# Kernel optimization log

Measured on AMD Instinct MI355X. Metric: run time of the kernel, lower is better.

## Reference

```python
import jax, jax.numpy as jnp
import numpy as np

D_MODEL = 1024
N_HEADS = 16
D_K = D_MODEL // N_HEADS  # 64
SCALE = 0.125             # attention_scale = 1/sqrt(d_k)
ROPE_BASE = 10000.0
NEG_INF = -1e30


def setup_inputs() -> dict:
    key = jax.random.key(0)
    k1, k2, k3 = jax.random.split(key, 3)
    B, S = 2, 2048
    x = jax.random.normal(k1, (B, S, D_MODEL), jnp.float32)
    # torch Linear(d_model, 3*d_model, bias=False): stored here as [in, out]
    w_qkv = jax.random.normal(k2, (D_MODEL, 3 * D_MODEL), jnp.float32) * (D_MODEL ** -0.5)
    w_o = jax.random.normal(k3, (D_MODEL, D_MODEL), jnp.float32) * (D_MODEL ** -0.5)
    return {"x": x, "w_qkv": w_qkv, "w_o": w_o}


def _rotary(x):
    # x: [B, H, S, D]; standard half-split rotary over sequence positions
    S, D = x.shape[2], x.shape[3]
    inv_freq = 1.0 / (ROPE_BASE ** (jnp.arange(0, D, 2, dtype=jnp.float32) / D))  # [D/2]
    freqs = jnp.arange(S, dtype=jnp.float32)[:, None] * inv_freq[None, :]          # [S, D/2]
    cos = jnp.cos(freqs)[None, None]  # [1,1,S,D/2]
    sin = jnp.sin(freqs)[None, None]
    x1, x2 = jnp.split(x, 2, axis=-1)
    return jnp.concatenate([x1 * cos + x2 * sin, -x1 * sin + x2 * cos], axis=-1).astype(x.dtype)


def reference(x, w_qkv, w_o):
    B, S, _ = x.shape
    qkv = x @ w_qkv                                        # [B,S,3*D_MODEL]
    qkv = qkv.reshape(B, S, 3, N_HEADS, D_K).transpose(2, 0, 3, 1, 4)  # [3,B,H,S,Dk]
    q, k, v = qkv[0], qkv[1], qkv[2]
    q = _rotary(q)
    k = _rotary(k)
    scores = jnp.einsum('bhqd,bhkd->bhqk', q, k) * SCALE   # [B,H,S,S]
    causal = jnp.tril(jnp.ones((S, S), dtype=bool))
    scores = jnp.where(causal, scores, NEG_INF)
    attn = jax.nn.softmax(scores, axis=-1)
    out = jnp.einsum('bhqk,bhkd->bhqd', attn, v)           # [B,H,S,Dk]
    out = out.transpose(0, 2, 1, 3).reshape(B, S, D_MODEL)
    return out @ w_o
```

## Files before the change

### kernel.cpp

```cpp
#include <hip/hip_runtime.h>

typedef short bf16x8 __attribute__((ext_vector_type(8)));
typedef short bf16x4 __attribute__((ext_vector_type(4)));
typedef float f32x4 __attribute__((ext_vector_type(4)));
typedef float f32x16 __attribute__((ext_vector_type(16)));
typedef int i32x4 __attribute__((ext_vector_type(4)));

#define DEVI static __device__ __forceinline__

DEVI unsigned short f2b(float f) {
  unsigned u = __float_as_uint(f);
  u += 0x7FFFu + ((u >> 16) & 1u);
  return (unsigned short)(u >> 16);
}

DEVI void gload16(const void* g, void* l) {
  __builtin_amdgcn_global_load_lds((const __attribute__((address_space(1))) void*)g,
                                   (__attribute__((address_space(3))) void*)l, 16, 0, 0);
}

DEVI void pl32swap(int a, int b, int& outa, int& outb) {
#if __has_builtin(__builtin_amdgcn_permlane32_swap)
  auto r = __builtin_amdgcn_permlane32_swap(a, b, false, false);
  outa = ((const int*)&r)[0];
  outb = ((const int*)&r)[1];
#else
  int bp = __shfl_xor(b, 32);
  int ap = __shfl_xor(a, 32);
  outa = (threadIdx.x & 32) ? bp : a;
  outb = (threadIdx.x & 32) ? b : ap;
#endif
}

DEVI float halfmax(float x) {
  int o0, o1;
  pl32swap(__float_as_int(x), __float_as_int(x), o0, o1);
  return fmaxf(__int_as_float(o0), __int_as_float(o1));
}
DEVI float halfsum(float x) {
  int o0, o1;
  pl32swap(__float_as_int(x), __float_as_int(x), o0, o1);
  return __int_as_float(o0) + __int_as_float(o1);
}

__global__ void rope_table_kernel(float2* __restrict__ cst) {
  int i = blockIdx.x * 256 + threadIdx.x;
  int s = i >> 5, j = i & 31;
  float inv = powf(10000.0f, -(float)j * (1.0f / 32.0f));
  float a = (float)s * inv;
  cst[i] = make_float2(cosf(a), sinf(a));
}

__global__ void cvt_x_kernel(const float* __restrict__ x, unsigned short* __restrict__ xb) {
  int i = blockIdx.x * 256 + threadIdx.x;
  float4 v = ((const float4*)x)[i];
  ushort4 o;
  o.x = f2b(v.x); o.y = f2b(v.y); o.z = f2b(v.z); o.w = f2b(v.w);
  ((ushort4*)xb)[i] = o;
}

__global__ void transpose2_kernel(const float* __restrict__ W1, unsigned short* __restrict__ WT1,
                                  const float* __restrict__ W2, unsigned short* __restrict__ WT2) {
  __shared__ float tile[32][33];
  int bx = blockIdx.x;
  const float* W; unsigned short* WT; int N;
  if (bx < 96) { W = W1; WT = WT1; N = 3072; }
  else         { W = W2; WT = WT2; N = 1024; bx -= 96; }
  const int K = 1024;
  int n0 = bx * 32, k0 = blockIdx.y * 32;
  int tx = threadIdx.x, ty = threadIdx.y;
#pragma unroll
  for (int i = 0; i < 32; i += 8)
    tile[ty + i][tx] = W[(size_t)(k0 + ty + i) * N + n0 + tx];
  __syncthreads();
#pragma unroll
  for (int i = 0; i < 32; i += 8)
    WT[(size_t)(n0 + ty + i) * K + k0 + tx] = f2b(tile[tx][ty + i]);
}

DEVI void gemm_mainloop(const unsigned short* __restrict__ A, const unsigned short* __restrict__ B,
                        unsigned short* As, unsigned short* Bs,
                        int m0, int n0, int lane, int wid, int wr, int wc,
                        f32x4 acc[4][4]) {
  const int srow = lane >> 3;
  const int scc = ((lane & 7) ^ srow) * 8;
  const int rx = lane & 7;
  auto stage = [&](int k0, int nb) {
    unsigned short* Ad = As + nb * 8192;
    unsigned short* Bd = Bs + nb * 8192;
#pragma unroll
    for (int i = 0; i < 4; ++i) {
      const int c = i * 4 + wid;
      const int row = c * 8 + srow;
      gload16(A + (size_t)(m0 + row) * 1024 + k0 + scc, (char*)Ad + c * 1024);
      gload16(B + (size_t)(n0 + row) * 1024 + k0 + scc, (char*)Bd + c * 1024);
    }
  };
  auto compute = [&](int nb) {
    const unsigned short* Ab = As + nb * 8192;
    const unsigned short* Bb = Bs + nb * 8192;
#pragma unroll
    for (int kk = 0; kk < 64; kk += 32) {
      const int cc = (((kk >> 3) + (lane >> 4)) ^ rx) * 8;
      bf16x8 a[4], b[4];
#pragma unroll
      for (int mi = 0; mi < 4; ++mi)
        a[mi] = *(const bf16x8*)&Ab[(wr * 64 + mi * 16 + (lane & 15)) * 64 + cc];
#pragma unroll
      for (int ni = 0; ni < 4; ++ni)
        b[ni] = *(const bf16x8*)&Bb[(wc * 64 + ni * 16 + (lane & 15)) * 64 + cc];
      __builtin_amdgcn_s_setprio(1);
#pragma unroll
      for (int mi = 0; mi < 4; ++mi)
#pragma unroll
        for (int ni = 0; ni < 4; ++ni)
          acc[mi][ni] = __builtin_amdgcn_mfma_f32_16x16x32_bf16(a[mi], b[ni], acc[mi][ni], 0, 0, 0);
      __builtin_amdgcn_s_setprio(0);
    }
  };
  stage(0, 0);
  stage(64, 1);
  for (int t = 0; t < 15; ++t) {
    asm volatile("s_waitcnt vmcnt(8)" ::: "memory");
    __builtin_amdgcn_s_barrier();
    compute(t & 1);
    __builtin_amdgcn_s_barrier();
    if (t < 14) stage((t + 2) * 64, t & 1);
  }
  asm volatile("s_waitcnt vmcnt(0)" ::: "memory");
  __builtin_amdgcn_s_barrier();
  compute(1);
}

__global__ __launch_bounds__(256, 2) void gemm_qkv_kernel(
    const unsigned short* __restrict__ Xb, const unsigned short* __restrict__ WT,
    const float2* __restrict__ cst,
    unsigned short* __restrict__ Qb, unsigned short* __restrict__ KT,
    unsigned short* __restrict__ VT) {
  __shared__ unsigned short As[2][8192];
  __shared__ unsigned short Bs[2][8192];
  const int lane = threadIdx.x & 63, wid = threadIdx.x >> 6;
  const int flat = blockIdx.y * 24 + blockIdx.x;
  const int nf = (flat & 7) * 96 + (flat >> 3);
  const int bx = nf % 24, by = nf / 24;
  const int m0 = by * 128, n0 = bx * 128;
  const int wr = wid >> 1, wc = wid & 1;
  f32x4 acc[4][4] = {};
  gemm_mainloop(Xb, WT, &As[0][0], &Bs[0][0], m0, n0, lane, wid, wr, wc, acc);

  __syncthreads();
  unsigned short* slab = (unsigned short*)((char*)&As[0][0] + wid * 8192);
  const int n_base = n0 + wc * 64;
  const int ty = n_base >> 10;
  const int h = (n_base & 1023) >> 6;
  const int qrow = (lane >> 4) << 2;
  const int l15 = lane & 15;
  const int rowg = m0 + wr * 64;
  const int s_half = rowg & 2047, bb = rowg >> 11;
  const int t_ = s_half >> 6;
  const size_t hb = (size_t)(bb * 16 + h) * 131072;

  if (ty == 0) {
#pragma unroll
    for (int mi = 0; mi < 4; ++mi) {
      const int rl0 = mi * 16 + qrow;
#pragma unroll
      for (int r = 0; r < 4; ++r) {
#pragma unroll
        for (int ni = 0; ni < 2; ++ni) {
          const int j = ni * 16 + l15;
          const float2 cs = cst[(s_half + rl0 + r) * 32 + j];
          const float x1 = acc[mi][ni][r], x2 = acc[mi][ni + 2][r];
          slab[(rl0 + r) * 64 + j]      = f2b(x1 * cs.x + x2 * cs.y);
          slab[(rl0 + r) * 64 + j + 32] = f2b(-x1 * cs.y + x2 * cs.x);
        }
      }
    }
    unsigned short* dst = Qb + hb + (size_t)s_half * 64;
#pragma unroll
    for (int i = 0; i < 8; ++i) {
      const int idx = i * 64 + lane;
      *(bf16x8*)&dst[idx * 8] = *(const bf16x8*)&slab[idx * 8];
    }
  } else if (ty == 1) {
#pragma unroll
    for (int mi = 0; mi < 4; ++mi) {
      const int rl0 = mi * 16 + qrow;
#pragma unroll
      for (int r = 0; r < 4; ++r) {
        const int row = rl0 + r;
#pragma unroll
        for (int ni = 0; ni < 2; ++ni) {
          const int j = ni * 16 + l15;
          const float2 cs = cst[(s_half + row) * 32 + j];
          const float x1 = acc[mi][ni][r], x2 = acc[mi][ni + 2][r];
          const int c = j >> 3, jr = j & 7;
          slab[c * 512 + row * 8 + jr]       = f2b(x1 * cs.x + x2 * cs.y);
          slab[(c + 4) * 512 + row * 8 + jr] = f2b(-x1 * cs.y + x2 * cs.x);
        }
      }
    }
    unsigned short* dst = KT + hb + (size_t)t_ * 4096;
#pragma unroll
    for (int i = 0; i < 8; ++i) {
      const int idx = i * 64 + lane;
      *(bf16x8*)&dst[idx * 8] = *(const bf16x8*)&slab[idx * 8];
    }
  } else {
#pragma unroll
    for (int mi = 0; mi < 4; ++mi) {
      const int rl0 = mi * 16 + qrow;
#pragma unroll
      for (int ni = 0; ni < 4; ++ni) {
        const int d = ni * 16 + l15;
#pragma unroll
        for (int r = 0; r < 4; ++r) {
          const int rl = rl0 + r;
          slab[(rl >> 3) * 512 + d * 8 + (rl & 7)] = f2b(acc[mi][ni][r]);
        }
      }
    }
    unsigned short* dst = VT + hb + (size_t)t_ * 4096;
#pragma unroll
    for (int i = 0; i < 8; ++i) {
      const int idx = i * 64 + lane;
      *(bf16x8*)&dst[idx * 8] = *(const bf16x8*)&slab[idx * 8];
    }
  }
}

DEVI void build_pa(const f32x16& s, bf16x8& pa0, bf16x8& pa1) {
  int cw[8];
#pragma unroll
  for (int i = 0; i < 8; ++i)
    asm("v_cvt_pk_bf16_f32 %0, %1, %2" : "=v"(cw[i]) : "v"(s[2 * i]), "v"(s[2 * i + 1]));
  int a0, a1, b0, b1, a2, a3, b2, b3;
  pl32swap(cw[0], cw[2], a0, b0);
  pl32swap(cw[1], cw[3], a1, b1);
  pl32swap(cw[4], cw[6], a2, b2);
  pl32swap(cw[5], cw[7], a3, b3);
  pa0 = __builtin_bit_cast(bf16x8, (i32x4){a0, a1, b0, b1});
  pa1 = __builtin_bit_cast(bf16x8, (i32x4){a2, a3, b2, b3});
}

DEVI void attn_pair(const unsigned char* __restrict__ kb, const unsigned char* __restrict__ vb,
                    const bf16x8 qf[4], int kglob, bool diag1, int qg, int ln, int hi,
                    float& m2, float& l_run, f32x16& acc0, f32x16& acc1) {
  const float C = 0.125f * 1.44269504f;
  f32x16 s0 = {}, s1 = {};
  {
    const unsigned char* kbase = kb + hi * 1024 + ln * 16;
    bf16x8 k0[4], k1[4];
#pragma unroll
    for (int j = 0; j < 4; ++j) {
      k0[j] = *(const bf16x8*)(kbase + j * 2048);
      k1[j] = *(const bf16x8*)(kbase + j * 2048 + 512);
    }
    __builtin_amdgcn_s_setprio(1);
#pragma unroll
    for (int j = 0; j < 4; ++j) {
      s0 = __builtin_amdgcn_mfma_f32_32x32x16_bf16(k0[j], qf[j], s0, 0, 0, 0);
      s1 = __builtin_amdgcn_mfma_f32_32x32x16_bf16(k1[j], qf[j], s1, 0, 0, 0);
    }
    __builtin_amdgcn_s_setprio(0);
  }
  bf16x8 va[2][2], vbf[2][2];
  {
    const unsigned char* vbase = vb + hi * 1024 + ln * 16;
#pragma unroll
    for (int st = 0; st < 2; ++st)
#pragma unroll
      for (int p = 0; p < 2; ++p) {
        va[st][p]  = *(const bf16x8*)(vbase + (4 * st + 2 * p) * 1024);
        vbf[st][p] = *(const bf16x8*)(vbase + (4 * st + 2 * p) * 1024 + 512);
      }
  }

  if (diag1) {
#pragma unroll
    for (int r = 0; r < 16; ++r) {
      const int kg = kglob + 32 + (r & 3) + ((r >> 2) << 3) + (hi << 2);
      if (kg > qg) s1[r] = -1e30f;
    }
  }
  float mraw = fmaxf(s0[0], s1[0]);
#pragma unroll
  for (int r = 1; r < 16; ++r) mraw = fmaxf(mraw, fmaxf(s0[r], s1[r]));
  const float mlc = mraw * C;
  if (__any(mlc > m2 + 11.5416f)) {
    const float mnew = fmaxf(m2, halfmax(mlc));
    const float sc = exp2f(m2 - mnew);
    l_run *= sc;
#pragma unroll
    for (int r = 0; r < 16; ++r) { acc0[r] *= sc; acc1[r] *= sc; }
    m2 = mnew;
  }
  float ps0 = 0.f, ps1 = 0.f;
#pragma unroll
  for (int r = 0; r < 16; ++r) { s0[r] = exp2f(fmaf(s0[r], C, -m2)); ps0 += s0[r]; }
#pragma unroll
  for (int r = 0; r < 16; ++r) { s1[r] = exp2f(fmaf(s1[r], C, -m2)); ps1 += s1[r]; }
  l_run += ps0 + ps1;

  bf16x8 pa[2][2];
  build_pa(s0, pa[0][0], pa[0][1]);
  build_pa(s1, pa[1][0], pa[1][1]);

  __builtin_amdgcn_s_setprio(1);
#pragma unroll
  for (int st = 0; st < 2; ++st) {
    acc0 = __builtin_amdgcn_mfma_f32_32x32x16_bf16(va[st][0], pa[st][0], acc0, 0, 0, 0);
    acc1 = __builtin_amdgcn_mfma_f32_32x32x16_bf16(vbf[st][0], pa[st][0], acc1, 0, 0, 0);
    acc0 = __builtin_amdgcn_mfma_f32_32x32x16_bf16(va[st][1], pa[st][1], acc0, 0, 0, 0);
    acc1 = __builtin_amdgcn_mfma_f32_32x32x16_bf16(vbf[st][1], pa[st][1], acc1, 0, 0, 0);
  }
  __builtin_amdgcn_s_setprio(0);
}

DEVI void attn_single(const unsigned char* __restrict__ kb, const unsigned char* __restrict__ vb,
                      const bf16x8 qf[4], int kglob, int qg, int ln, int hi,
                      float& m2, float& l_run, f32x16& acc0, f32x16& acc1) {
  const float C = 0.125f * 1.44269504f;
  f32x16 s0 = {};
  {
    const unsigned char* kbase = kb + hi * 1024 + ln * 16;
    bf16x8 k0[4];
#pragma unroll
    for (int j = 0; j < 4; ++j) k0[j] = *(const bf16x8*)(kbase + j * 2048);
    __builtin_amdgcn_s_setprio(1);
#pragma unroll
    for (int j = 0; j < 4; ++j)
      s0 = __builtin_amdgcn_mfma_f32_32x32x16_bf16(k0[j], qf[j], s0, 0, 0, 0);
    __builtin_amdgcn_s_setprio(0);
  }
  bf16x8 va[2], vbf[2];
  {
    const unsigned char* vbase = vb + hi * 1024 + ln * 16;
#pragma unroll
    for (int p = 0; p < 2; ++p) {
      va[p]  = *(const bf16x8*)(vbase + (2 * p) * 1024);
      vbf[p] = *(const bf16x8*)(vbase + (2 * p) * 1024 + 512);
    }
  }
#pragma unroll
  for (int r = 0; r < 16; ++r) {
    const int kg = kglob + (r & 3) + ((r >> 2) << 3) + (hi << 2);
    if (kg > qg) s0[r] = -1e30f;
  }
  float mraw = s0[0];
#pragma unroll
  for (int r = 1; r < 16; ++r) mraw = fmaxf(mraw, s0[r]);
  const float mlc = mraw * C;
  if (__any(mlc > m2 + 11.5416f)) {
    const float mnew = fmaxf(m2, halfmax(mlc));
    const float sc = exp2f(m2 - mnew);
    l_run *= sc;
#pragma unroll
    for (int r = 0; r < 16; ++r) { acc0[r] *= sc; acc1[r] *= sc; }
    m2 = mnew;
  }
  float ps = 0.f;
#pragma unroll
  for (int r = 0; r < 16; ++r) { s0[r] = exp2f(fmaf(s0[r], C, -m2)); ps += s0[r]; }
  l_run += ps;

  bf16x8 pa0, pa1;
  build_pa(s0, pa0, pa1);
  __builtin_amdgcn_s_setprio(1);
  acc0 = __builtin_amdgcn_mfma_f32_32x32x16_bf16(va[0], pa0, acc0, 0, 0, 0);
  acc1 = __builtin_amdgcn_mfma_f32_32x32x16_bf16(vbf[0], pa0, acc1, 0, 0, 0);
  acc0 = __builtin_amdgcn_mfma_f32_32x32x16_bf16(va[1], pa1, acc0, 0, 0, 0);
  acc1 = __builtin_amdgcn_mfma_f32_32x32x16_bf16(vbf[1], pa1, acc1, 0, 0, 0);
  __builtin_amdgcn_s_setprio(0);
}

__global__ __launch_bounds__(512, 2) void attn_kernel(
    const unsigned short* __restrict__ Qb, const unsigned short* __restrict__ KT,
    const unsigned short* __restrict__ VT, unsigned short* __restrict__ Ob) {
  const int tid = threadIdx.x;
  const int lane = tid & 63, wid = tid >> 6;
  const int ln = lane & 31, hi = lane >> 5;
  const int s = wid & 3, half = wid >> 2;
  const int bh = blockIdx.x;
  const int p = blockIdx.y;
  const int j = half ? p : (15 - p);
  const int q0 = j * 128 + s * 32;
  const int qg = q0 + ln;
  const int top = q0 >> 5;
  const unsigned short* Qh = Qb + (size_t)bh * 131072;
  const unsigned char* KTb = (const unsigned char*)(KT + (size_t)bh * 131072);
  const unsigned char* VTb = (const unsigned char*)(VT + (size_t)bh * 131072);

  bf16x8 qf[4];
  {
    const unsigned short* pq = Qh + (size_t)(q0 + ln) * 64 + hi * 8;
#pragma unroll
    for (int t = 0; t < 4; ++t) qf[t] = *(const bf16x8*)(pq + t * 16);
  }

  f32x16 acc0 = {}, acc1 = {};
  float m2 = -1e30f, l_run = 0.f;
  const int ntile = (top >> 1) + 1;

  for (int t = 0; t < ntile; ++t) {
    const unsigned char* kb = KTb + (size_t)t * 8192;
    const unsigned char* vb = VTb + (size_t)t * 8192;
    const int nv = top - 2 * t + 1;
    if (nv >= 2)
      attn_pair(kb, vb, qf, t * 64, top == 2 * t + 1, qg, ln, hi, m2, l_run, acc0, acc1);
    else
      attn_single(kb, vb, qf, t * 64, qg, ln, hi, m2, l_run, acc0, acc1);
  }
  l_run = halfsum(l_run);

  const float il = 1.0f / l_run;
  const int b = bh >> 4, h = bh & 15;
  unsigned short* ob = Ob + ((size_t)(b * 2048 + qg)) * 1024 + h * 64;
#pragma unroll
  for (int g = 0; g < 4; ++g) {
    ushort4 o0, o1;
    o0.x = f2b(acc0[4 * g + 0] * il); o0.y = f2b(acc0[4 * g + 1] * il);
    o0.z = f2b(acc0[4 * g + 2] * il); o0.w = f2b(acc0[4 * g + 3] * il);
    o1.x = f2b(acc1[4 * g + 0] * il); o1.y = f2b(acc1[4 * g + 1] * il);
    o1.z = f2b(acc1[4 * g + 2] * il); o1.w = f2b(acc1[4 * g + 3] * il);
    *(ushort4*)&ob[8 * g + 4 * hi]      = o0;
    *(ushort4*)&ob[32 + 8 * g + 4 * hi] = o1;
  }
}

__global__ __launch_bounds__(256) void gemm_out_kernel(
    const unsigned short* __restrict__ Ob, const unsigned short* __restrict__ WoT,
    float* __restrict__ out) {
  __shared__ unsigned short As[2][8192];
  __shared__ unsigned short Bs[2][8192];
  const int lane = threadIdx.x & 63, wid = threadIdx.x >> 6;
  const int m0 = blockIdx.y * 128, n0 = blockIdx.x * 128;
  const int wr = wid >> 1, wc = wid & 1;
  f32x4 acc[4][4] = {};
  gemm_mainloop(Ob, WoT, &As[0][0], &Bs[0][0], m0, n0, lane, wid, wr, wc, acc);
#pragma unroll
  for (int mi = 0; mi < 4; ++mi) {
    const int mrow = m0 + wr * 64 + mi * 16 + ((lane >> 4) << 2);
#pragma unroll
    for (int ni = 0; ni < 4; ++ni) {
      const int n = n0 + wc * 64 + ni * 16 + (lane & 15);
#pragma unroll
      for (int r = 0; r < 4; ++r)
        out[(size_t)(mrow + r) * 1024 + n] = acc[mi][ni][r];
    }
  }
}

extern "C" void kernel_launch(void* const* d_in, const int* in_sizes, int n_in,
                              void* d_out, int out_size, void* d_ws, size_t ws_size,
                              hipStream_t stream) {
  const float* x     = (const float*)d_in[0];
  const float* w_qkv = (const float*)d_in[1];
  const float* w_o   = (const float*)d_in[2];
  float* out = (float*)d_out;
  char* ws = (char*)d_ws;

  const size_t MB = 1 << 20;
  float2* cst = (float2*)(ws);
  unsigned short* Xb  = (unsigned short*)(ws + (512 << 10));
  unsigned short* WqT = (unsigned short*)(ws + (512 << 10) + 8  * MB);
  unsigned short* WoT = (unsigned short*)(ws + (512 << 10) + 14 * MB);
  unsigned short* Qb  = (unsigned short*)(ws + (512 << 10) + 16 * MB);
  unsigned short* KT  = (unsigned short*)(ws + (512 << 10) + 24 * MB);
  unsigned short* VT  = (unsigned short*)(ws + (512 << 10) + 32 * MB);
  unsigned short* Ob  = Xb;

  rope_table_kernel<<<dim3(256), dim3(256), 0, stream>>>(cst);
  cvt_x_kernel<<<dim3(4096), dim3(256), 0, stream>>>(x, Xb);
  transpose2_kernel<<<dim3(128, 32), dim3(32, 8), 0, stream>>>(w_qkv, WqT, w_o, WoT);
  gemm_qkv_kernel<<<dim3(24, 32), dim3(256), 0, stream>>>(Xb, WqT, cst, Qb, KT, VT);
  attn_kernel<<<dim3(32, 8), dim3(512), 0, stream>>>(Qb, KT, VT, Ob);
  gemm_out_kernel<<<dim3(8, 32), dim3(256), 0, stream>>>(Ob, WoT, out);
}
```

Baseline: 123.5 us.

## Split KV tiles across four wave groups per query block with LDS merge

Doubles the attention block to 16 waves and splits each query block's KV tiles round-robin across four wave groups. Partial softmax states (m, l, accumulators) are combined through shared memory in a tree of synchronized merges before writing output. The two causal halves are now processed in sequence within the block. The goal is to shorten the per-wave critical path and raise waves per CU. In exchange it adds barriers, LDS traffic and register pressure from the tighter launch bounds.

```diff
diff --git a/kernel.cpp b/kernel.cpp
--- a/kernel.cpp
+++ b/kernel.cpp
@@ -374,57 +374,102 @@
   __builtin_amdgcn_s_setprio(0);
 }
 
-__global__ __launch_bounds__(512, 2) void attn_kernel(
+DEVI void write_partial(float* M, int slot, const f32x16& a0, const f32x16& a1,
+                        float m2, float l) {
+#pragma unroll
+  for (int r = 0; r < 16; ++r) { M[slot + r] = a0[r]; M[slot + 16 + r] = a1[r]; }
+  M[slot + 32] = m2;
+  M[slot + 33] = l;
+}
+
+DEVI void merge_state(const float* M, int slot, float& m, float& l,
+                      f32x16& a0, f32x16& a1) {
+  const float mp = M[slot + 32], lp = M[slot + 33];
+  const float mn = fmaxf(m, mp);
+  const float eo = exp2f(m - mn), ep = exp2f(mp - mn);
+  l = l * eo + lp * ep;
+#pragma unroll
+  for (int r = 0; r < 16; ++r) {
+    a0[r] = a0[r] * eo + M[slot + r] * ep;
+    a1[r] = a1[r] * eo + M[slot + 16 + r] * ep;
+  }
+  m = mn;
+}
+
+DEVI void writeO(unsigned short* __restrict__ Ob, const f32x16& a0, const f32x16& a1,
+                 float l, int bh, int q0, int ln, int hi) {
+  const float il = 1.0f / l;
+  const int b = bh >> 4, h = bh & 15;
+  unsigned short* ob = Ob + ((size_t)(b * 2048 + q0 + ln)) * 1024 + h * 64;
+#pragma unroll
+  for (int g = 0; g < 4; ++g) {
+    ushort4 o0, o1;
+    o0.x = f2b(a0[4 * g + 0] * il); o0.y = f2b(a0[4 * g + 1] * il);
+    o0.z = f2b(a0[4 * g + 2] * il); o0.w = f2b(a0[4 * g + 3] * il);
+    o1.x = f2b(a1[4 * g + 0] * il); o1.y = f2b(a1[4 * g + 1] * il);
+    o1.z = f2b(a1[4 * g + 2] * il); o1.w = f2b(a1[4 * g + 3] * il);
+    *(ushort4*)&ob[8 * g + 4 * hi]      = o0;
+    *(ushort4*)&ob[32 + 8 * g + 4 * hi] = o1;
+  }
+}
+
+__global__ __launch_bounds__(1024, 4) void attn_kernel(
     const unsigned short* __restrict__ Qb, const unsigned short* __restrict__ KT,
     const unsigned short* __restrict__ VT, unsigned short* __restrict__ Ob) {
+  __shared__ float M[8704];
   const int tid = threadIdx.x;
   const int lane = tid & 63, wid = tid >> 6;
   const int ln = lane & 31, hi = lane >> 5;
-  const int s = wid & 3, half = wid >> 2;
+  const int s = wid & 3, r = wid >> 2;
   const int bh = blockIdx.x;
   const int p = blockIdx.y;
-  const int j = half ? p : (15 - p);
-  const int q0 = j * 128 + s * 32;
-  const int qg = q0 + ln;
-  const int top = q0 >> 5;
   const unsigned short* Qh = Qb + (size_t)bh * 131072;
   const unsigned char* KTb = (const unsigned char*)(KT + (size_t)bh * 131072);
   const unsigned char* VTb = (const unsigned char*)(VT + (size_t)bh * 131072);
-
-  bf16x8 qf[4];
-  {
-    const unsigned short* pq = Qh + (size_t)(q0 + ln) * 64 + hi * 8;
-#pragma unroll
-    for (int t = 0; t < 4; ++t) qf[t] = *(const bf16x8*)(pq + t * 16);
-  }
-
-  f32x16 acc0 = {}, acc1 = {};
-  float m2 = -1e30f, l_run = 0.f;
-  const int ntile = (top >> 1) + 1;
-
-  for (int t = 0; t < ntile; ++t) {
-    const unsigned char* kb = KTb + (size_t)t * 8192;
-    const unsigned char* vb = VTb + (size_t)t * 8192;
-    const int nv = top - 2 * t + 1;
-    if (nv >= 2)
-      attn_pair(kb, vb, qf, t * 64, top == 2 * t + 1, qg, ln, hi, m2, l_run, acc0, acc1);
-    else
-      attn_single(kb, vb, qf, t * 64, qg, ln, hi, m2, l_run, acc0, acc1);
-  }
-  l_run = halfsum(l_run);
-
-  const float il = 1.0f / l_run;
-  const int b = bh >> 4, h = bh & 15;
-  unsigned short* ob = Ob + ((size_t)(b * 2048 + qg)) * 1024 + h * 64;
-#pragma unroll
-  for (int g = 0; g < 4; ++g) {
-    ushort4 o0, o1;
-    o0.x = f2b(acc0[4 * g + 0] * il); o0.y = f2b(acc0[4 * g + 1] * il);
-    o0.z = f2b(acc0[4 * g + 2] * il); o0.w = f2b(acc0[4 * g + 3] * il);
-    o1.x = f2b(acc1[4 * g + 0] * il); o1.y = f2b(acc1[4 * g + 1] * il);
-    o1.z = f2b(acc1[4 * g + 2] * il); o1.w = f2b(acc1[4 * g + 3] * il);
-    *(ushort4*)&ob[8 * g + 4 * hi]      = o0;
-    *(ushort4*)&ob[32 + 8 * g + 4 * hi] = o1;
+  const int slot = (s * 64 + lane) * 34;
+
+  for (int phase = 0; phase < 2; ++phase) {
+    const int j = phase ? p : (15 - p);
+    const int q0 = j * 128 + s * 32;
+    const int qg = q0 + ln;
+    const int top = q0 >> 5;
+    const int maxT = top >> 1;
+
+    bf16x8 qf[4];
+    {
+      const unsigned short* pq = Qh + (size_t)(q0 + ln) * 64 + hi * 8;
+#pragma unroll
+      for (int t = 0; t < 4; ++t) qf[t] = *(const bf16x8*)(pq + t * 16);
+    }
+    f32x16 a0 = {}, a1 = {};
+    float m2 = -1e30f, l = 0.f;
+
+    for (int t = r; t <= maxT; t += 4) {
+      const unsigned char* kb = KTb + (size_t)t * 8192;
+      const unsigned char* vb = VTb + (size_t)t * 8192;
+      const int nv = top - 2 * t + 1;
+      if (nv >= 2)
+        attn_pair(kb, vb, qf, t * 64, top == 2 * t + 1, qg, ln, hi, m2, l, a0, a1);
+      else
+        attn_single(kb, vb, qf, t * 64, qg, ln, hi, m2, l, a0, a1);
+    }
+    l = halfsum(l);
+
+    __syncthreads();
+    if (r == 1) write_partial(M, slot, a0, a1, m2, l);
+    __syncthreads();
+    if (r == 0) merge_state(M, slot, m2, l, a0, a1);
+    __syncthreads();
+    if (r == 3) write_partial(M, slot, a0, a1, m2, l);
+    __syncthreads();
+    if (r == 2) merge_state(M, slot, m2, l, a0, a1);
+    __syncthreads();
+    if (r == 2) write_partial(M, slot, a0, a1, m2, l);
+    __syncthreads();
+    if (r == 0) {
+      merge_state(M, slot, m2, l, a0, a1);
+      writeO(Ob, a0, a1, l, bh, q0, ln, hi);
+    }
   }
 }
 
@@ -474,6 +519,6 @@
   cvt_x_kernel<<<dim3(4096), dim3(256), 0, stream>>>(x, Xb);
   transpose2_kernel<<<dim3(128, 32), dim3(32, 8), 0, stream>>>(w_qkv, WqT, w_o, WoT);
   gemm_qkv_kernel<<<dim3(24, 32), dim3(256), 0, stream>>>(Xb, WqT, cst, Qb, KT, VT);
-  attn_kernel<<<dim3(32, 8), dim3(512), 0, stream>>>(Qb, KT, VT, Ob);
+  attn_kernel<<<dim3(32, 8), dim3(1024), 0, stream>>>(Qb, KT, VT, Ob);
   gemm_out_kernel<<<dim3(8, 32), dim3(256), 0, stream>>>(Ob, WoT, out);
 }
```

Result: slower. 132.7 us (+7.4%).

## Prefetch K fragments across tiles and split attention into 256-thread blocks

Applied to the files above, without the earlier changes.

The attention loop now double-buffers K fragments in registers, issuing the next tile's K loads right after the current QK MFMAs so load latency overlaps softmax and PV work. The separate single-subtile path is removed, and the final partial tile is handled by the pair path with full causal masking. The launch changes from 512-thread blocks that paired a heavy and a light query block to 256-thread blocks over a 32x16 grid, heaviest first, with launch bounds raised to 3 blocks per CU. This trades explicit load pairing and some wasted masked compute for more blocks, better latency hiding and somewhat higher register pressure.

```diff
diff --git a/kernel.cpp b/kernel.cpp
--- a/kernel.cpp
+++ b/kernel.cpp
@@ -229,6 +229,17 @@
   }
 }
 
+struct KF { bf16x8 a[4], b[4]; };
+
+DEVI void loadK(const unsigned char* kb, int ln, int hi, KF& K) {
+  const unsigned char* kbase = kb + hi * 1024 + ln * 16;
+#pragma unroll
+  for (int j = 0; j < 4; ++j) {
+    K.a[j] = *(const bf16x8*)(kbase + j * 2048);
+    K.b[j] = *(const bf16x8*)(kbase + j * 2048 + 512);
+  }
+}
+
 DEVI void build_pa(const f32x16& s, bf16x8& pa0, bf16x8& pa1) {
   int cw[8];
 #pragma unroll
@@ -243,27 +254,21 @@
   pa1 = __builtin_bit_cast(bf16x8, (i32x4){a2, a3, b2, b3});
 }
 
-DEVI void attn_pair(const unsigned char* __restrict__ kb, const unsigned char* __restrict__ vb,
-                    const bf16x8 qf[4], int kglob, bool diag1, int qg, int ln, int hi,
+DEVI void attn_tile(const KF& K, KF& Kn, const unsigned char* nkb, int doPre,
+                    const unsigned char* vb, const bf16x8 qf[4], int kglob,
+                    int masked, int qg, int ln, int hi,
                     float& m2, float& l_run, f32x16& acc0, f32x16& acc1) {
   const float C = 0.125f * 1.44269504f;
   f32x16 s0 = {}, s1 = {};
-  {
-    const unsigned char* kbase = kb + hi * 1024 + ln * 16;
-    bf16x8 k0[4], k1[4];
-#pragma unroll
-    for (int j = 0; j < 4; ++j) {
-      k0[j] = *(const bf16x8*)(kbase + j * 2048);
-      k1[j] = *(const bf16x8*)(kbase + j * 2048 + 512);
-    }
-    __builtin_amdgcn_s_setprio(1);
-#pragma unroll
-    for (int j = 0; j < 4; ++j) {
-      s0 = __builtin_amdgcn_mfma_f32_32x32x16_bf16(k0[j], qf[j], s0, 0, 0, 0);
-      s1 = __builtin_amdgcn_mfma_f32_32x32x16_bf16(k1[j], qf[j], s1, 0, 0, 0);
-    }
-    __builtin_amdgcn_s_setprio(0);
-  }
+  __builtin_amdgcn_s_setprio(1);
+#pragma unroll
+  for (int j = 0; j < 4; ++j) {
+    s0 = __builtin_amdgcn_mfma_f32_32x32x16_bf16(K.a[j], qf[j], s0, 0, 0, 0);
+    s1 = __builtin_amdgcn_mfma_f32_32x32x16_bf16(K.b[j], qf[j], s1, 0, 0, 0);
+  }
+  __builtin_amdgcn_s_setprio(0);
+  if (doPre) loadK(nkb, ln, hi, Kn);
+
   bf16x8 va[2][2], vbf[2][2];
   {
     const unsigned char* vbase = vb + hi * 1024 + ln * 16;
@@ -276,11 +281,12 @@
       }
   }
 
-  if (diag1) {
+  if (masked) {
 #pragma unroll
     for (int r = 0; r < 16; ++r) {
-      const int kg = kglob + 32 + (r & 3) + ((r >> 2) << 3) + (hi << 2);
-      if (kg > qg) s1[r] = -1e30f;
+      const int kg = kglob + (r & 3) + ((r >> 2) << 3) + (hi << 2);
+      if (kg > qg) s0[r] = -1e30f;
+      if (kg + 32 > qg) s1[r] = -1e30f;
     }
   }
   float mraw = fmaxf(s0[0], s1[0]);
@@ -317,76 +323,18 @@
   __builtin_amdgcn_s_setprio(0);
 }
 
-DEVI void attn_single(const unsigned char* __restrict__ kb, const unsigned char* __restrict__ vb,
-                      const bf16x8 qf[4], int kglob, int qg, int ln, int hi,
-                      float& m2, float& l_run, f32x16& acc0, f32x16& acc1) {
-  const float C = 0.125f * 1.44269504f;
-  f32x16 s0 = {};
-  {
-    const unsigned char* kbase = kb + hi * 1024 + ln * 16;
-    bf16x8 k0[4];
-#pragma unroll
-    for (int j = 0; j < 4; ++j) k0[j] = *(const bf16x8*)(kbase + j * 2048);
-    __builtin_amdgcn_s_setprio(1);
-#pragma unroll
-    for (int j = 0; j < 4; ++j)
-      s0 = __builtin_amdgcn_mfma_f32_32x32x16_bf16(k0[j], qf[j], s0, 0, 0, 0);
-    __builtin_amdgcn_s_setprio(0);
-  }
-  bf16x8 va[2], vbf[2];
-  {
-    const unsigned char* vbase = vb + hi * 1024 + ln * 16;
-#pragma unroll
-    for (int p = 0; p < 2; ++p) {
-      va[p]  = *(const bf16x8*)(vbase + (2 * p) * 1024);
-      vbf[p] = *(const bf16x8*)(vbase + (2 * p) * 1024 + 512);
-    }
-  }
-#pragma unroll
-  for (int r = 0; r < 16; ++r) {
-    const int kg = kglob + (r & 3) + ((r >> 2) << 3) + (hi << 2);
-    if (kg > qg) s0[r] = -1e30f;
-  }
-  float mraw = s0[0];
-#pragma unroll
-  for (int r = 1; r < 16; ++r) mraw = fmaxf(mraw, s0[r]);
-  const float mlc = mraw * C;
-  if (__any(mlc > m2 + 11.5416f)) {
-    const float mnew = fmaxf(m2, halfmax(mlc));
-    const float sc = exp2f(m2 - mnew);
-    l_run *= sc;
-#pragma unroll
-    for (int r = 0; r < 16; ++r) { acc0[r] *= sc; acc1[r] *= sc; }
-    m2 = mnew;
-  }
-  float ps = 0.f;
-#pragma unroll
-  for (int r = 0; r < 16; ++r) { s0[r] = exp2f(fmaf(s0[r], C, -m2)); ps += s0[r]; }
-  l_run += ps;
-
-  bf16x8 pa0, pa1;
-  build_pa(s0, pa0, pa1);
-  __builtin_amdgcn_s_setprio(1);
-  acc0 = __builtin_amdgcn_mfma_f32_32x32x16_bf16(va[0], pa0, acc0, 0, 0, 0);
-  acc1 = __builtin_amdgcn_mfma_f32_32x32x16_bf16(vbf[0], pa0, acc1, 0, 0, 0);
-  acc0 = __builtin_amdgcn_mfma_f32_32x32x16_bf16(va[1], pa1, acc0, 0, 0, 0);
-  acc1 = __builtin_amdgcn_mfma_f32_32x32x16_bf16(vbf[1], pa1, acc1, 0, 0, 0);
-  __builtin_amdgcn_s_setprio(0);
-}
-
-__global__ __launch_bounds__(512, 2) void attn_kernel(
+__global__ __launch_bounds__(256, 3) void attn_kernel(
     const unsigned short* __restrict__ Qb, const unsigned short* __restrict__ KT,
     const unsigned short* __restrict__ VT, unsigned short* __restrict__ Ob) {
   const int tid = threadIdx.x;
   const int lane = tid & 63, wid = tid >> 6;
   const int ln = lane & 31, hi = lane >> 5;
-  const int s = wid & 3, half = wid >> 2;
   const int bh = blockIdx.x;
-  const int p = blockIdx.y;
-  const int j = half ? p : (15 - p);
-  const int q0 = j * 128 + s * 32;
+  const int j = 15 - (int)blockIdx.y;
+  const int q0 = j * 128 + wid * 32;
   const int qg = q0 + ln;
   const int top = q0 >> 5;
+  const int nt = (top >> 1) + 1;
   const unsigned short* Qh = Qb + (size_t)bh * 131072;
   const unsigned char* KTb = (const unsigned char*)(KT + (size_t)bh * 131072);
   const unsigned char* VTb = (const unsigned char*)(VT + (size_t)bh * 131072);
@@ -400,17 +348,23 @@
 
   f32x16 acc0 = {}, acc1 = {};
   float m2 = -1e30f, l_run = 0.f;
-  const int ntile = (top >> 1) + 1;
-
-  for (int t = 0; t < ntile; ++t) {
-    const unsigned char* kb = KTb + (size_t)t * 8192;
-    const unsigned char* vb = VTb + (size_t)t * 8192;
-    const int nv = top - 2 * t + 1;
-    if (nv >= 2)
-      attn_pair(kb, vb, qf, t * 64, top == 2 * t + 1, qg, ln, hi, m2, l_run, acc0, acc1);
-    else
-      attn_single(kb, vb, qf, t * 64, qg, ln, hi, m2, l_run, acc0, acc1);
-  }
+
+  KF KA, KB;
+  loadK(KTb, ln, hi, KA);
+  int t = 0;
+  while (t + 2 <= nt) {
+    attn_tile(KA, KB, KTb + (size_t)(t + 1) * 8192, 1, VTb + (size_t)t * 8192,
+              qf, t * 64, 0, qg, ln, hi, m2, l_run, acc0, acc1);
+    const int last2 = (t + 2 == nt);
+    attn_tile(KB, KA, KTb + (last2 ? 0 : (size_t)(t + 2) * 8192), !last2,
+              VTb + (size_t)(t + 1) * 8192, qf, (t + 1) * 64, last2, qg, ln, hi,
+              m2, l_run, acc0, acc1);
+    t += 2;
+  }
+  if (t < nt)
+    attn_tile(KA, KB, KTb, 0, VTb + (size_t)t * 8192, qf, t * 64, 1, qg, ln, hi,
+              m2, l_run, acc0, acc1);
+
   l_run = halfsum(l_run);
 
   const float il = 1.0f / l_run;
@@ -474,6 +428,6 @@
   cvt_x_kernel<<<dim3(4096), dim3(256), 0, stream>>>(x, Xb);
   transpose2_kernel<<<dim3(128, 32), dim3(32, 8), 0, stream>>>(w_qkv, WqT, w_o, WoT);
   gemm_qkv_kernel<<<dim3(24, 32), dim3(256), 0, stream>>>(Xb, WqT, cst, Qb, KT, VT);
-  attn_kernel<<<dim3(32, 8), dim3(512), 0, stream>>>(Qb, KT, VT, Ob);
+  attn_kernel<<<dim3(32, 16), dim3(256), 0, stream>>>(Qb, KT, VT, Ob);
   gemm_out_kernel<<<dim3(8, 32), dim3(256), 0, stream>>>(Ob, WoT, out);
 }
```

Result: slower. 195.2 us (+58.0%).
